# Kernel optimization log

Hardware: AMD Instinct MI355X
Metric: run time of the kernel (lower is better)

Reference implementation:

```python
import jax, jax.numpy as jnp
import numpy as np

BETA1, BETA2, BETA3 = 0.9, 0.8, 0.9
DECAY1, INC1 = 0.05, 5.0
DECAY3, INC3 = 0.05, 5.0
LATENCY = 4.0
B_CONST = 0.15
LIF1_MIN, LIF1_MAX = 150.0, 400.0
LIF3_MIN, LIF3_MAX = 50.0, 200.0
A_P, A_M, TAU_P, TAU_M = 0.01, 0.01, 20.0, 20.0  # exponential STDP params (params1/2/3)


def stdp(dt):
    # exponential STDP curve: potentiate when post fires after pre (dt>=0), depress otherwise
    return jnp.where(dt >= 0, A_P * jnp.exp(-dt / TAU_P), -A_M * jnp.exp(dt / TAU_M))


def setup_inputs() -> dict:
    key = jax.random.key(0)
    k1, k2, k3, k4 = jax.random.split(key, 4)
    H, N, C = 8192, 4096, 128
    return {
        "image": jax.random.uniform(k1, (N,), jnp.float32),
        "W1": jax.random.uniform(k2, (H, N), jnp.float32),
        "W2": jax.random.uniform(k3, (N, H), jnp.float32),
        "W3": jax.random.uniform(k4, (C, N), jnp.float32),
        "thr1": 100.0 * jnp.ones((H,), jnp.float32),
        "thr2": 5.0 * jnp.ones((N,), jnp.float32),
        "thr3": 100.0 * jnp.ones((C,), jnp.float32),
        "time": 256,
        "pw": 8,
    }


def reference(image, W1, W2, W3, thr1, thr2, thr3, time, pw):
    N = image.shape[0]
    H = W1.shape[0]
    C = W3.shape[0]
    T = int(time)
    Tf = jnp.float32(T)

    img_t = Tf * image  # input spike times, [N]
    # rate -> pulse encoding: input_spikes[t, i] = 1 for t in [floor(img_t[i]), floor(img_t[i])+pw)
    t_axis = jnp.arange(T, dtype=jnp.float32)[:, None]          # [T,1]
    start = jnp.floor(img_t)[None, :]                            # [1,N]
    input_spikes = ((t_axis >= start) & (t_axis < start + pw)).astype(jnp.float32)  # [T,N]

    def wta(mem, th):
        # winner-take-all (snntorch inhibition=True): only argmax neuron may spike
        j = jnp.argmax(mem)
        fire = (mem[j] > th[j]).astype(mem.dtype)
        return fire * jax.nn.one_hot(j, mem.shape[0], dtype=mem.dtype)

    def step(carry, xs):
        mem1, mem2, mem3, th1, th3, r1, r2, r3, hid_act, out_act = carry
        x, t = xs
        # layer 1: Leaky LIF, inhibition, reset-to-zero
        mem1 = BETA1 * mem1 + jnp.dot(W1, x)
        spk1 = wta(mem1, th1)
        mem1 = mem1 * (1.0 - spk1)
        # layer 2: Leaky LIF, no inhibition, reset-by-subtract
        mem2 = BETA2 * mem2 + jnp.dot(W2, spk1)
        spk2 = (mem2 > thr2).astype(mem2.dtype)
        mem2 = mem2 - spk2 * thr2
        # layer 3 (clustering): Leaky LIF, inhibition, zeroed after any spike
        mem3 = BETA3 * mem3 + jnp.dot(W3, spk2)
        spk3 = wta(mem3, th3)
        mem3 = mem3 - spk3 * th3
        mem3 = jnp.where(jnp.sum(spk3) > 0, 0.0, mem3)
        # first-spike-time recon (recon stays at first nonzero spk*(t+1))
        r1 = jnp.where(r1 != 0, r1, spk1 * (t + 1.0))
        r2 = jnp.where(r2 != 0, r2, spk2 * (t + 1.0))
        r3 = jnp.where(r3 != 0, r3, spk3 * (t + 1.0))
        hid_act = hid_act + spk1
        out_act = out_act + spk2
        # adaptive thresholds: homeostatic decay + spike-triggered increase, clamped
        th1 = jnp.clip(th1 - DECAY1 + INC1 * spk1, LIF1_MIN, LIF1_MAX)
        th3 = jnp.clip(th3 - DECAY3 + INC3 * spk3, LIF3_MIN, LIF3_MAX)
        return (mem1, mem2, mem3, th1, th3, r1, r2, r3, hid_act, out_act), None

    z = jnp.zeros
    carry0 = (z(H), z(N), z(C), thr1, thr3, z(H), z(N), z(C), z(H), z(N))
    (mem1, mem2, mem3, th1, th3, r1, r2, r3, hid_act, out_act), _ = jax.lax.scan(
        step, carry0, (input_spikes, jnp.arange(T, dtype=jnp.float32)))

    # neurons that never spiked get time T
    r1 = jnp.where(r1 == 0, Tf, r1)
    r2 = jnp.where(r2 == 0, Tf, r2)
    r3 = jnp.where(r3 == 0, Tf, r3)

    # STDP weight updates (exponential), same structure as PresentImage
    hid_mask = (hid_act > 0).astype(jnp.float32)
    delta_t1 = (r1[:, None] - img_t[None, :]) * hid_mask[:, None]      # [H,N]
    W1_new = W1 + stdp(delta_t1)
    delta_t2 = r2[:, None] - r1[None, :]                                # [N,H]
    zeta = (Tf - r1) * hid_mask / Tf                                    # [H]
    rho = (r2 - LATENCY - img_t) / Tf + B_CONST                         # [N]
    W2_new = jnp.clip(W2 + stdp(delta_t2) * (rho[:, None] * zeta[None, :]), 0.0, 1.0)
    delta_t3 = r3[:, None] - r2[None, :]                                # [C,N]
    W3_new = W3 + stdp(delta_t3)

    error = (img_t - (r2 - LATENCY)) / Tf
    error_scalar = jnp.sum(jnp.square(error))
    return (error, error_scalar, r1, r2, r3, W1_new, W2_new, W3_new)
```

## Files before the change

### kernel.cpp

```cpp
#include <hip/hip_runtime.h>
#include <cstdint>
#include <cstddef>

#define Hn 8192
#define Nn 4096
#define Cn 128
#define Tt 256
#define CAP 192

typedef unsigned long long ull;

__device__ __forceinline__ float th_lazy2(float b, float lo, float hi, int nup){
    if (nup <= 0) return b;
    float a = fminf(fmaxf(__fsub_rn(b, 0.05f), lo), hi);
    if (nup == 1) return a;
    return fmaxf(__fsub_rn(a, __fmul_rn(0.05f, (float)(nup - 1))), lo);
}

__device__ __forceinline__ float clamp01(float v){
    return fminf(fmaxf(v, 0.f), 1.f);
}

template<int CTRL>
__device__ __forceinline__ int dpp_i(int x, int old){
    return __builtin_amdgcn_update_dpp(old, x, CTRL, 0xf, 0xf, false);
}
__device__ __forceinline__ float wave_max_f(float v){
    const int NEG = __float_as_int(-3.4e38f);
#define STEPM(C) { float o = __int_as_float(dpp_i<C>(__float_as_int(v), NEG)); v = fmaxf(v, o); }
    STEPM(0x111) STEPM(0x112) STEPM(0x114) STEPM(0x118) STEPM(0x142) STEPM(0x143)
#undef STEPM
    return __int_as_float(__builtin_amdgcn_readlane(__float_as_int(v), 63));
}
__device__ __forceinline__ int wave_argmax_l(float bv, int bh, float &wv, int &wh){
    float v = wave_max_f(bv);
    ull tie = __ballot(bv == v);
    int tl = __ffsll((long long)tie) - 1;
    int h = __builtin_amdgcn_readlane(bh, tl);
    if (__builtin_expect(__popcll(tie) > 1, 0)){
        ull m = tie & (tie - 1);
        while (m){
            int l2 = __ffsll((long long)m) - 1;
            int h2 = __builtin_amdgcn_readlane(bh, l2);
            if (h2 < h){ h = h2; tl = l2; }
            m &= m - 1;
        }
    }
    wv = v; wh = h; return tl;
}
__device__ __forceinline__ float rl_f(float x, int l){
    return __int_as_float(__builtin_amdgcn_readlane(__float_as_int(x), l));
}

__global__ __launch_bounds__(1024) void k_prep(const float* __restrict__ image,
        int* __restrict__ boff, int* __restrict__ sidx, unsigned* __restrict__ anyv){
    __shared__ int s_start[Nn];
    __shared__ int s_c4[4][Tt];
    __shared__ int s_boff[Tt + 1];
    int tid = threadIdx.x;
    for (int i = tid; i < Nn; i += 1024)
        s_start[i] = (int)floorf(__fmul_rn(256.f, image[i]));
    if (tid < Tt) anyv[tid] = 0u;
    __syncthreads();
    int b = tid & 255, q = tid >> 8;
    {
        int c = 0;
        for (int k = 0; k < 1024; ++k) c += (s_start[q * 1024 + k] == b) ? 1 : 0;
        s_c4[q][b] = c;
    }
    __syncthreads();
    if (tid == 0){
        int acc = 0;
        for (int bb = 0; bb < Tt; ++bb){
            s_boff[bb] = acc;
            acc += s_c4[0][bb] + s_c4[1][bb] + s_c4[2][bb] + s_c4[3][bb];
        }
        s_boff[Tt] = acc;
    }
    __syncthreads();
    if (tid <= Tt) boff[tid] = s_boff[tid];
    int p = s_boff[b];
    if (q > 0) p += s_c4[0][b];
    if (q > 1) p += s_c4[1][b];
    if (q > 2) p += s_c4[2][b];
    for (int k = 0; k < 1024; ++k){
        int i = q * 1024 + k;
        if (s_start[i] == b) sidx[p++] = i;
    }
}

__global__ __launch_bounds__(256) void k_gbuckets(const float* __restrict__ W1,
        const int* __restrict__ boff, const int* __restrict__ sidx,
        float* __restrict__ G_T){
    __shared__ float rows[2][Nn];
    int tid = threadIdx.x;
    int h0 = blockIdx.x * 2;
    for (int r = 0; r < 2; ++r){
        const float4* src = (const float4*)(W1 + (size_t)(h0 + r) * Nn);
        float4* dst = (float4*)rows[r];
        for (int j = tid; j < Nn / 4; j += 256) dst[j] = src[j];
    }
    __syncthreads();
    int t = tid;
    int b0 = boff[t], b1 = boff[t + 1];
    float s0 = 0.f, s1 = 0.f;
    for (int k = b0; k < b1; ++k){
        int i = sidx[k];
        s0 += rows[0][i]; s1 += rows[1][i];
    }
    G_T[(size_t)(h0 + 0) * Tt + t] = s0;
    G_T[(size_t)(h0 + 1) * Tt + t] = s1;
}

__global__ __launch_bounds__(256) void k_c1M(const float* __restrict__ G_T,
        float* __restrict__ M, float* __restrict__ r1pre, float* __restrict__ o_r1){
    __shared__ float tile[32][Tt + 1];
    __shared__ float c1s[32][Tt + 1];
    const int tid = threadIdx.x;
    const int h0 = blockIdx.x * 32;
    for (int r = 0; r < 32; ++r) tile[r][tid] = G_T[(size_t)(h0 + r) * Tt + tid];
    __syncthreads();
    {
        int hs = tid & 31, ts = tid >> 5;
        for (int tb = 0; tb < 32; ++tb){
            int t = tb * 8 + ts;
            int lo = (t - 7 < 0) ? 0 : t - 7;
            float s = 0.f;
            for (int u = lo; u <= t; ++u) s += tile[hs][u];
            c1s[hs][t] = s;
        }
    }
    __syncthreads();
    if (tid < 32){
        float m = 0.f;
        for (int t = 0; t < Tt; ++t){
            m = __fadd_rn(__fmul_rn(0.9f, m), c1s[tid][t]);
            M[(size_t)t * Hn + h0 + tid] = m;
        }
        r1pre[h0 + tid] = 0.f;
        o_r1[h0 + tid] = 256.f;
    }
}

__global__ __launch_bounds__(256) void k_sel(const float* __restrict__ M,
        float4* __restrict__ cand){
    const int t = blockIdx.x, tid = threadIdx.x;
    __shared__ float s_row[Hn];
    __shared__ unsigned s_hist[256];
    __shared__ unsigned s_suf[256];
    __shared__ unsigned s_pref;
    __shared__ int s_rank;
    __shared__ int s_cnt;
    __shared__ int s_idx[CAP + 64];
    {
        const float4* src = (const float4*)(M + (size_t)t * Hn);
        float4* d4 = (float4*)s_row;
        for (int j = tid; j < Hn / 4; j += 256) d4[j] = src[j];
    }
    if (tid == 0){ s_pref = 0u; s_rank = CAP; s_cnt = 0; }
    __syncthreads();
#pragma unroll
    for (int b = 3; b >= 0; --b){
        s_hist[tid] = 0u;
        __syncthreads();
        unsigned pref = s_pref;
        int r = s_rank;
        for (int k = 0; k < 32; ++k){
            unsigned u = __float_as_uint(s_row[tid + (k << 8)]);
            bool match = (b == 3) ? true : ((u >> ((b + 1) * 8)) == pref);
            if (match) atomicAdd(&s_hist[(u >> (b * 8)) & 255], 1u);
        }
        __syncthreads();
        s_suf[tid] = s_hist[tid];
        __syncthreads();
#pragma unroll
        for (int off = 1; off < 256; off <<= 1){
            unsigned v = (tid + off < 256) ? s_suf[tid + off] : 0u;
            __syncthreads();
            s_suf[tid] += v;
            __syncthreads();
        }
        unsigned above = s_suf[tid] - s_hist[tid];
        if ((int)above < r && r <= (int)s_suf[tid]){
            s_pref = (pref << 8) | (unsigned)tid;
            s_rank = r - (int)above;
        }
        __syncthreads();
    }
    unsigned V = s_pref;
    for (int k = 0; k < 32; ++k){
        int i = tid + (k << 8);
        unsigned u = __float_as_uint(s_row[i]);
        if (u >= V){
            int p = atomicAdd(&s_cnt, 1);
            if (p < CAP + 64) s_idx[p] = i;
        }
    }
    __syncthreads();
    int c = s_cnt;
    bool ovf = (c > CAP);
    float vV = ovf ? 3.4e38f : __uint_as_float(V);
    for (int i = tid; i < CAP; i += 256){
        float4 e;
        if (!ovf && i < c){
            int ix = s_idx[i];
            e = make_float4(s_row[ix], __int_as_float(ix | (1 << 15)), 0.f, vV);
        } else {
            e = make_float4(-1.f, 0.f, 0.f, vV);
        }
        cand[(size_t)t * CAP + i] = e;
    }
}

#define NB_W1 1024
#define NB_W2 1024
#define NB_W3T 128

union FusedLDS {
    struct {
        float off[Hn];
        float thb[Hn];
        unsigned char ts[Hn];
        int j1[Tt];
        unsigned bm[256];
    } w;
    float tl[64][65];
};

__global__ __launch_bounds__(512, 1) void k_fused(
        const float* __restrict__ M, const float4* __restrict__ cand,
        const float* __restrict__ thr1,
        const float* __restrict__ W1, const float* __restrict__ W2,
        const float* __restrict__ W3,
        float* __restrict__ o_W1, float* __restrict__ o_W2, float* __restrict__ W3T,
        float* __restrict__ r1pre, float* __restrict__ o_r1,
        int* __restrict__ j1s, int* __restrict__ mh, int* __restrict__ nRout){
    __shared__ FusedLDS u;
    const int bid = blockIdx.x;
    const int tid = threadIdx.x;

    if (bid >= 1 && bid < 1 + NB_W1){
        size_t base = (size_t)(bid - 1) * 8192;
        const float4* src = (const float4*)W1;
        float4* dst = (float4*)o_W1;
        for (int i = tid; i < 8192; i += 512){
            float4 s = src[base + i];
            s.x = __fadd_rn(s.x, 0.01f); s.y = __fadd_rn(s.y, 0.01f);
            s.z = __fadd_rn(s.z, 0.01f); s.w = __fadd_rn(s.w, 0.01f);
            dst[base + i] = s;
        }
        return;
    }
    if (bid >= 1 + NB_W1 && bid < 1 + NB_W1 + NB_W2){
        size_t base = (size_t)(bid - 1 - NB_W1) * 8192;
        const float4* src = (const float4*)W2;
        float4* dst = (float4*)o_W2;
        for (int i = tid; i < 8192; i += 512){
            float4 s = src[base + i];
            s.x = clamp01(s.x); s.y = clamp01(s.y);
            s.z = clamp01(s.z); s.w = clamp01(s.w);
            dst[base + i] = s;
        }
        return;
    }
    if (bid >= 1 + NB_W1 + NB_W2){
        int r = bid - 1 - NB_W1 - NB_W2;
        int bx = r & 63, by = r >> 6;
        int n0 = bx * 64, c0 = by * 64;
        for (int e = tid; e < 64 * 64; e += 512){
            int rr = e >> 6, cc = e & 63;
            u.tl[rr][cc] = W3[(size_t)(c0 + rr) * Nn + n0 + cc];
        }
        __syncthreads();
        for (int e = tid; e < 64 * 64; e += 512){
            int rn = e >> 6, cc = e & 63;
            W3T[(size_t)(n0 + rn) * Cn + c0 + cc] = u.tl[cc][rn];
        }
        return;
    }

    for (int h = tid; h < Hn; h += 512){
        u.w.off[h] = 0.f;
        u.w.thb[h] = thr1[h];
        u.w.ts[h] = 0;
    }
    __syncthreads();
    if (tid >= 64) return;
    const int lane = tid;
    const float Lc = -0.15200309344504997f;

    float4 cA0 = cand[lane],         cA1 = cand[64 + lane],         cA2 = cand[128 + lane];
    float4 cB0 = cand[CAP + lane],   cB1 = cand[CAP + 64 + lane],   cB2 = cand[CAP + 128 + lane];
    float4 cC0 = cand[2*CAP + lane], cC1 = cand[2*CAP + 64 + lane], cC2 = cand[2*CAP + 128 + lane];
    float gofA0, gofA1, gofA2, gtsA0, gtsA1, gtsA2, gthA0, gthA1, gthA2;
#define GATHA(c) { int hh = __float_as_int(cA##c.y) & 8191; \
        gofA##c = u.w.off[hh]; gtsA##c = (float)u.w.ts[hh] - 1.f; gthA##c = u.w.thb[hh]; }
    GATHA(0) GATHA(1) GATHA(2)
#undef GATHA

    for (int t = 0; t < Tt; ++t){
        const float tf = (float)t;
        float bm = -3.4e38f; int bhh = 0x7FFFFFFF;
        float braw = 0.f, bts = 0.f, bthb = 0.f;
#define CPROC(c) { \
        int mc = __float_as_int(cA##c.y); \
        int hc = mc & 8191; \
        float dd = __fsub_rn(tf, gtsA##c); \
        float mem = __fsub_rn(cA##c.x, __fmul_rn(exp2f(__fmul_rn(dd, Lc)), gofA##c)); \
        if (!((mc >> 15) & 1)) mem = -3.4e38f; \
        if (mem > bm || (mem == bm && hc < bhh)){ bm = mem; bhh = hc; braw = cA##c.x; bts = gtsA##c; bthb = gthA##c; } }
        CPROC(0) CPROC(1) CPROC(2)
#undef CPROC
        int hB0 = __float_as_int(cB0.y) & 8191;
        int hB1 = __float_as_int(cB1.y) & 8191;
        int hB2 = __float_as_int(cB2.y) & 8191;
        float gofB0 = u.w.off[hB0], gtsB0 = (float)u.w.ts[hB0] - 1.f, gthB0 = u.w.thb[hB0];
        float gofB1 = u.w.off[hB1], gtsB1 = (float)u.w.ts[hB1] - 1.f, gthB1 = u.w.thb[hB1];
        float gofB2 = u.w.off[hB2], gtsB2 = (float)u.w.ts[hB2] - 1.f, gthB2 = u.w.thb[hB2];
        float wv; int wh;
        int wl = wave_argmax_l(bm, bhh, wv, wh);
        float raw = rl_f(braw, wl), tsv = rl_f(bts, wl), thb = rl_f(bthb, wl);
        const float vc = cA0.w;
        int skip = 0;
        if (__builtin_expect(wv < vc, 0)){
            if (t > 0 && vc < 150.f){
                skip = 1;
            } else {
                float fv = -3.4e38f; int fh = 0x7FFFFFFF;
                float fraw = 0.f, fts = 0.f, fthb = 0.f;
                const float4* Mrow4 = (const float4*)(M + (size_t)t * Hn);
                for (int q = 0; q < 32; ++q){
                    int e = q * 64 + lane;
                    float4 mv = Mrow4[e];
                    int ib = e * 4;
#define FPROC(comp, o2) { float x = mv.comp; int h2 = ib + o2; \
                    float gts = (float)u.w.ts[h2] - 1.f; \
                    float dd = __fsub_rn(tf, gts); \
                    float mm = __fsub_rn(x, __fmul_rn(exp2f(__fmul_rn(dd, Lc)), u.w.off[h2])); \
                    if (mm > fv || (mm == fv && h2 < fh)){ fv = mm; fh = h2; fraw = x; fts = gts; fthb = u.w.thb[h2]; } }
                    FPROC(x, 0) FPROC(y, 1) FPROC(z, 2) FPROC(w, 3)
#undef FPROC
                }
                wl = wave_argmax_l(fv, fh, wv, wh);
                raw = rl_f(fraw, wl); tsv = rl_f(fts, wl); fthb = rl_f(fthb, wl); thb = fthb;
            }
        }
        int fire = 0; float thnew = 0.f;
        if (!skip){
            float te = th_lazy2(thb, 150.f, 400.f, t - (int)tsv - 1);
            if (wv > te){
                fire = 1;
                thnew = fminf(fmaxf(__fadd_rn(__fsub_rn(te, 0.05f), 5.0f), 150.f), 400.f);
            }
        }
        if (fire){
            if (lane == 0){
                u.w.j1[t] = wh;
                j1s[t] = wh;
                if (tsv < 0.f){ o_r1[wh] = tf + 1.f; r1pre[wh] = tf + 1.f; }
                u.w.off[wh] = raw;
                u.w.ts[wh] = (unsigned char)((t + 1 < 256) ? (t + 1) : 255);
                u.w.thb[wh] = thnew;
            }
            if (hB0 == wh){ gofB0 = raw; gtsB0 = tf; gthB0 = thnew; }
            if (hB1 == wh){ gofB1 = raw; gtsB1 = tf; gthB1 = thnew; }
            if (hB2 == wh){ gofB2 = raw; gtsB2 = tf; gthB2 = thnew; }
        } else {
            if (lane == 0){ u.w.j1[t] = -1; j1s[t] = -1; }
        }
        cA0 = cB0; cA1 = cB1; cA2 = cB2;
        cB0 = cC0; cB1 = cC1; cB2 = cC2;
        int tn = (t + 3 < Tt) ? t + 3 : Tt - 1;
        cC0 = cand[(size_t)tn * CAP + lane];
        cC1 = cand[(size_t)tn * CAP + 64 + lane];
        cC2 = cand[(size_t)tn * CAP + 128 + lane];
        gofA0 = gofB0; gtsA0 = gtsB0; gthA0 = gthB0;
        gofA1 = gofB1; gtsA1 = gtsB1; gthA1 = gthB1;
        gofA2 = gofB2; gtsA2 = gtsB2; gthA2 = gthB2;
    }

    for (int i = lane; i < 256; i += 64) u.w.bm[i] = 0u;
    asm volatile("s_waitcnt lgkmcnt(0)" ::: "memory");
    for (int i = lane; i < Tt; i += 64){
        int h = u.w.j1[i];
        if (h >= 0) atomicOr(&u.w.bm[h >> 5], 1u << (h & 31));
    }
    asm volatile("s_waitcnt lgkmcnt(0)" ::: "memory");
    unsigned w0 = u.w.bm[lane*4+0], w1 = u.w.bm[lane*4+1];
    unsigned w2 = u.w.bm[lane*4+2], w3 = u.w.bm[lane*4+3];
    int c = __popc(w0) + __popc(w1) + __popc(w2) + __popc(w3);
    int inc = c;
#pragma unroll
    for (int off = 1; off < 64; off <<= 1){
        int v = __shfl_up(inc, off);
        if (lane >= off) inc += v;
    }
    int b = inc - c;
#define WALK(wrd, k) { unsigned ww = wrd; while (ww){ int bt = __ffs(ww) - 1; ww &= ww - 1; \
        mh[b++] = ((lane * 4 + k) << 5) | bt; } }
    WALK(w0, 0) WALK(w1, 1) WALK(w2, 2) WALK(w3, 3)
#undef WALK
    if (lane == 63) *nRout = inc;
}

__global__ __launch_bounds__(64) void k_lif2(const float* __restrict__ W2,
        const int* __restrict__ j1s, const float* __restrict__ thr2,
        float* __restrict__ o_r2, ull* __restrict__ spkb, unsigned* __restrict__ anyv){
    __shared__ int s_j[Tt];
    int lane = threadIdx.x, blk = blockIdx.x;
    for (int i = lane; i < Tt; i += 64) s_j[i] = j1s[i];
    __syncthreads();
    int n = blk * 64 + lane;
    const float* Wrow = W2 + (size_t)n * Hn;
    float tv = thr2[n], m = 0.f, rp = 0.f;
#define LD(dst, tt) { int hh = s_j[tt]; dst = (hh >= 0) ? Wrow[hh] : 0.f; }
#define STEP(uu, tt) { m = __fadd_rn(__fmul_rn(0.8f, m), uu); int f = 0; \
        if (m > tv){ m = __fsub_rn(m, tv); if (rp == 0.f) rp = (float)((tt) + 1); f = 1; } \
        ull mask = __ballot(f); \
        if (lane == 0){ spkb[(tt) * 64 + blk] = mask; if (mask) atomicOr(&anyv[tt], 1u); } }
    float u0, u1, u2, u3;
    LD(u0, 0) LD(u1, 1) LD(u2, 2) LD(u3, 3)
    for (int g = 0; g < 64; ++g){
        float v0 = 0.f, v1 = 0.f, v2 = 0.f, v3 = 0.f;
        if (g < 63){
            int bb = (g + 1) * 4;
            LD(v0, bb) LD(v1, bb + 1) LD(v2, bb + 2) LD(v3, bb + 3)
        }
        int t = g * 4;
        STEP(u0, t) STEP(u1, t + 1) STEP(u2, t + 2) STEP(u3, t + 3)
        u0 = v0; u1 = v1; u2 = v2; u3 = v3;
    }
#undef LD
#undef STEP
    o_r2[n] = (rp == 0.f) ? 256.f : rp;
}

__global__ __launch_bounds__(128, 1) void k_sim3(const ull* __restrict__ spkb,
        const unsigned* __restrict__ anyv, const float* __restrict__ W3T,
        const float* __restrict__ thr3, float* __restrict__ o_r3){
    int tid = threadIdx.x, lane = tid & 63, w = tid >> 6;
    __shared__ unsigned s_any[Tt];
    __shared__ ull s_r2[2];
    __shared__ int s_fire;
    for (int i = tid; i < Tt; i += 128) s_any[i] = anyv[i];
    float m = 0.f, th0 = thr3[tid], rp = 0.f, thv = 0.f;
    int ts = -1, zero = 1;
    __syncthreads();
    for (int t = 0; t < Tt; ++t){
        if (zero && s_any[t] == 0u) continue;
        float d = 0.f;
        if (s_any[t]){
            for (int ww = 0; ww < 64; ++ww){
                ull bits = spkb[t * 64 + ww];
                while (bits){
                    int b2 = __ffsll((long long)bits) - 1;
                    bits &= bits - 1;
                    d = __fadd_rn(d, W3T[(size_t)(ww * 64 + b2) * Cn + tid]);
                }
            }
        }
        m = __fadd_rn(__fmul_rn(0.9f, m), d);
        ull k = (((ull)__float_as_uint(m >= 0.f ? m : 0.f)) << 32) | (unsigned)(8191 - tid);
        if (!(m >= 0.f)) k = (unsigned)(8191 - tid);
#pragma unroll
        for (int off = 32; off >= 1; off >>= 1){
            ull o = __shfl_down(k, off);
            if (o > k) k = o;
        }
        if (lane == 0) s_r2[w] = k;
        __syncthreads();
        ull wk = s_r2[0] > s_r2[1] ? s_r2[0] : s_r2[1];
        int wc = 8191 - (int)(wk & 0xFFFFu);
        float wv = __uint_as_float((unsigned)(wk >> 32));
        if (tid == wc){
            float te = (ts < 0) ? th_lazy2(th0, 50.f, 200.f, t)
                                : th_lazy2(thv, 50.f, 200.f, t - ts - 1);
            int f = (wv > te) ? 1 : 0;
            s_fire = f;
            if (f){
                thv = fminf(fmaxf(__fadd_rn(__fsub_rn(te, 0.05f), 5.0f), 50.f), 200.f);
                ts = t;
                if (rp == 0.f) rp = (float)(t + 1);
            }
        }
        __syncthreads();
        if (s_fire){ m = 0.f; zero = 1; }
        else zero = 0;
        __syncthreads();
    }
    o_r3[tid] = (rp == 0.f) ? 256.f : rp;
}

__global__ __launch_bounds__(1024) void k_scalars(const float* __restrict__ image,
        const float* __restrict__ r1pre, const float* __restrict__ o_r1,
        const float* __restrict__ o_r2,
        float* __restrict__ zeta, float* __restrict__ rho,
        float* __restrict__ imgt, float* __restrict__ eiP, float* __restrict__ eiM,
        float* __restrict__ Pv, float* __restrict__ Qv,
        float* __restrict__ E2P, float* __restrict__ E2M,
        float* __restrict__ o_err, float* __restrict__ o_es){
    int tid = threadIdx.x;
    for (int h = tid; h < Hn; h += 1024){
        float r1f = o_r1[h];
        float mask = (r1pre[h] != 0.f) ? 1.f : 0.f;
        float z = __fmul_rn(__fmul_rn(__fsub_rn(256.f, r1f), mask), 0.00390625f);
        zeta[h] = z;
        Pv[h] = __expf(r1f * 0.05f) * z;
        Qv[h] = __expf(-r1f * 0.05f) * z;
    }
    float acc = 0.f;
    for (int n = tid; n < Nn; n += 1024){
        float img = __fmul_rn(256.f, image[n]);
        float r2f = o_r2[n];
        float e = __fmul_rn(__fsub_rn(img, __fsub_rn(r2f, 4.0f)), 0.00390625f);
        o_err[n] = e;
        rho[n] = __fadd_rn(__fmul_rn(__fsub_rn(__fsub_rn(r2f, 4.0f), img), 0.00390625f), 0.15f);
        imgt[n] = img;
        eiP[n] = __expf(img * 0.05f);
        eiM[n] = __expf(-img * 0.05f);
        E2P[n] = __expf(r2f * 0.05f);
        E2M[n] = __expf(-r2f * 0.05f);
        acc = __fadd_rn(acc, __fmul_rn(e, e));
    }
    __shared__ float red[16];
    for (int off = 32; off >= 1; off >>= 1) acc += __shfl_down(acc, off);
    int lane = tid & 63, w = tid >> 6;
    if (lane == 0) red[w] = acc;
    __syncthreads();
    if (tid == 0){
        float s = 0.f;
        for (int q = 0; q < 16; ++q) s += red[q];
        *o_es = s;
    }
}

__global__ __launch_bounds__(256) void k_w1fix(const float* __restrict__ W1,
        const float* __restrict__ imgt, const float* __restrict__ eiP,
        const float* __restrict__ eiM, const float* __restrict__ o_r1,
        const int* __restrict__ mh, const int* __restrict__ nRout,
        float* __restrict__ o_W1){
    int slot = blockIdx.x;
    if (slot >= *nRout) return;
    int h = mh[slot];
    int tid = threadIdx.x;
    float r1f = o_r1[h];
    float a = 0.01f * __expf(-r1f * 0.05f);
    float b = 0.01f * __expf( r1f * 0.05f);
    const float4* src = (const float4*)(W1 + (size_t)h * Nn);
    float4* dst = (float4*)(o_W1 + (size_t)h * Nn);
    const float4* ig = (const float4*)imgt;
    const float4* p4 = (const float4*)eiP;
    const float4* m4 = (const float4*)eiM;
    for (int i = tid; i < Nn / 4; i += 256){
        float4 s = src[i];
        float4 im = ig[i], pp = p4[i], mm = m4[i];
        s.x += (r1f >= im.x) ? a * pp.x : -(b * mm.x);
        s.y += (r1f >= im.y) ? a * pp.y : -(b * mm.y);
        s.z += (r1f >= im.z) ? a * pp.z : -(b * mm.z);
        s.w += (r1f >= im.w) ? a * pp.w : -(b * mm.w);
        dst[i] = s;
    }
}

__global__ __launch_bounds__(128) void k_w2fix(
        const float* __restrict__ o_r1, const float* __restrict__ Pv,
        const float* __restrict__ Qv, const float* __restrict__ o_r2,
        const float* __restrict__ rho, const int* __restrict__ mh,
        const int* __restrict__ nRout, float* __restrict__ o_W2){
    __shared__ int   s_h[Tt];
    __shared__ float s_rv[Tt], s_pp[Tt], s_qq[Tt];
    int n = blockIdx.x, tid = threadIdx.x;
    int nRv = *nRout;
    for (int s = tid; s < nRv; s += 128){
        int h = mh[s];
        s_h[s] = h; s_rv[s] = o_r1[h]; s_pp[s] = Pv[h]; s_qq[s] = Qv[h];
    }
    __syncthreads();
    float r2f = o_r2[n], rh = rho[n];
    float A = 0.01f * rh * __expf(-r2f * 0.05f);
    float B = 0.01f * rh * __expf( r2f * 0.05f);
    for (int s = tid; s < nRv; s += 128){
        size_t idx = (size_t)n * Hn + s_h[s];
        float w = o_W2[idx];
        float rv = s_rv[s];
        w = clamp01(w + ((r2f >= rv) ? A * s_pp[s] : -(B * s_qq[s])));
        o_W2[idx] = w;
    }
}

__global__ __launch_bounds__(256) void k_w3new(const float* __restrict__ W3,
        const float* __restrict__ o_r2, const float* __restrict__ E2P,
        const float* __restrict__ E2M, const float* __restrict__ o_r3,
        float* __restrict__ o_W3){
    int c = blockIdx.x, tid = threadIdx.x;
    float r3f = o_r3[c];
    float a = 0.01f * __expf(-r3f * 0.05f);
    float b = 0.01f * __expf( r3f * 0.05f);
    const float4* src = (const float4*)(W3 + (size_t)c * Nn);
    float4* dst = (float4*)(o_W3 + (size_t)c * Nn);
    const float4* r24 = (const float4*)o_r2;
    const float4* p4 = (const float4*)E2P;
    const float4* m4 = (const float4*)E2M;
    for (int i = tid; i < Nn / 4; i += 256){
        float4 s = src[i]; float4 rv = r24[i]; float4 pp = p4[i]; float4 mm = m4[i];
        s.x += (r3f >= rv.x) ? a * pp.x : -(b * mm.x);
        s.y += (r3f >= rv.y) ? a * pp.y : -(b * mm.y);
        s.z += (r3f >= rv.z) ? a * pp.z : -(b * mm.z);
        s.w += (r3f >= rv.w) ? a * pp.w : -(b * mm.w);
        dst[i] = s;
    }
}

extern "C" void kernel_launch(void* const* d_in, const int* in_sizes, int n_in,
                              void* d_out, int out_size, void* d_ws, size_t ws_size,
                              hipStream_t stream){
    const float* image = (const float*)d_in[0];
    const float* W1   = (const float*)d_in[1];
    const float* W2   = (const float*)d_in[2];
    const float* W3   = (const float*)d_in[3];
    const float* thr1 = (const float*)d_in[4];
    const float* thr2 = (const float*)d_in[5];
    const float* thr3 = (const float*)d_in[6];

    float* out  = (float*)d_out;
    float* o_err = out;
    float* o_es  = out + 4096;
    float* o_r1  = out + 4097;
    float* o_r2  = out + 12289;
    float* o_r3  = out + 16385;
    float* o_W1  = out + 16513;
    float* o_W2  = o_W1 + (size_t)Hn * Nn;
    float* o_W3  = o_W2 + (size_t)Nn * Hn;

    float* ws = (float*)d_ws;
    float* G_T   = ws;
    float* M     = G_T + (size_t)Hn * Tt;
    float* W3T   = M + (size_t)Tt * Hn;
    float4* cand = (float4*)(W3T + (size_t)Nn * Cn);
    ull* spkb    = (ull*)(cand + (size_t)Tt * CAP);
    float* r1pre = (float*)(spkb + (size_t)Tt * 64);
    float* zeta  = r1pre + Hn;
    float* rho   = zeta + Hn;
    float* imgt  = rho + Nn;
    float* eiP   = imgt + Nn;
    float* eiM   = eiP + Nn;
    float* Pv    = eiM + Nn;
    float* Qv    = Pv + Hn;
    float* E2P   = Qv + Hn;
    float* E2M   = E2P + Nn;
    int* boff   = (int*)(E2M + Nn);
    int* sidx   = boff + (Tt + 1);
    int* j1s    = sidx + Nn;
    int* mh     = j1s + Tt;
    int* nRout  = mh + 256;
    unsigned* anyv = (unsigned*)(nRout + 1);

    k_prep<<<1, 1024, 0, stream>>>(image, boff, sidx, anyv);
    k_gbuckets<<<Hn / 2, 256, 0, stream>>>(W1, boff, sidx, G_T);
    k_c1M<<<Hn / 32, 256, 0, stream>>>(G_T, M, r1pre, o_r1);
    k_sel<<<Tt, 256, 0, stream>>>(M, cand);
    k_fused<<<1 + NB_W1 + NB_W2 + NB_W3T, 512, 0, stream>>>(
        M, cand, thr1, W1, W2, W3, o_W1, o_W2, W3T, r1pre, o_r1, j1s, mh, nRout);
    k_lif2<<<Nn / 64, 64, 0, stream>>>(W2, j1s, thr2, o_r2, spkb, anyv);
    k_sim3<<<1, 128, 0, stream>>>(spkb, anyv, W3T, thr3, o_r3);
    k_scalars<<<1, 1024, 0, stream>>>(image, r1pre, o_r1, o_r2, zeta, rho,
                                      imgt, eiP, eiM, Pv, Qv, E2P, E2M, o_err, o_es);
    k_w1fix<<<256, 256, 0, stream>>>(W1, imgt, eiP, eiM, o_r1, mh, nRout, o_W1);
    k_w2fix<<<Nn, 128, 0, stream>>>(o_r1, Pv, Qv, o_r2, rho, mh, nRout, o_W2);
    k_w3new<<<Cn, 256, 0, stream>>>(W3, o_r2, E2P, E2M, o_r3, o_W3);
}
```

Baseline: 542.1 us.

## Compact layer-1 neuron state into slot-indexed float4 table and shrink fused block

```diff
diff --git a/kernel.cpp b/kernel.cpp
--- a/kernel.cpp
+++ b/kernel.cpp
@@ -143,7 +143,7 @@
 }
 
 __global__ __launch_bounds__(256) void k_sel(const float* __restrict__ M,
-        float4* __restrict__ cand){
+        const float* __restrict__ thr1, float4* __restrict__ cand){
     const int t = blockIdx.x, tid = threadIdx.x;
     __shared__ float s_row[Hn];
     __shared__ unsigned s_hist[256];
@@ -204,7 +204,7 @@
         float4 e;
         if (!ovf && i < c){
             int ix = s_idx[i];
-            e = make_float4(s_row[ix], __int_as_float(ix | (1 << 15)), 0.f, vV);
+            e = make_float4(s_row[ix], __int_as_float(ix | (1 << 15)), thr1[ix], vV);
         } else {
             e = make_float4(-1.f, 0.f, 0.f, vV);
         }
@@ -212,22 +212,21 @@
     }
 }
 
-#define NB_W1 1024
-#define NB_W2 1024
+#define NB_W1 2048
+#define NB_W2 2048
 #define NB_W3T 128
 
 union FusedLDS {
     struct {
-        float off[Hn];
-        float thb[Hn];
-        unsigned char ts[Hn];
+        unsigned short slot[Hn];
+        float4 fst[260];
         int j1[Tt];
         unsigned bm[256];
     } w;
     float tl[64][65];
 };
 
-__global__ __launch_bounds__(512, 1) void k_fused(
+__global__ __launch_bounds__(256, 1) void k_fused(
         const float* __restrict__ M, const float4* __restrict__ cand,
         const float* __restrict__ thr1,
         const float* __restrict__ W1, const float* __restrict__ W2,
@@ -240,10 +239,10 @@
     const int tid = threadIdx.x;
 
     if (bid >= 1 && bid < 1 + NB_W1){
-        size_t base = (size_t)(bid - 1) * 8192;
+        size_t base = (size_t)(bid - 1) * 4096;
         const float4* src = (const float4*)W1;
         float4* dst = (float4*)o_W1;
-        for (int i = tid; i < 8192; i += 512){
+        for (int i = tid; i < 4096; i += 256){
             float4 s = src[base + i];
             s.x = __fadd_rn(s.x, 0.01f); s.y = __fadd_rn(s.y, 0.01f);
             s.z = __fadd_rn(s.z, 0.01f); s.w = __fadd_rn(s.w, 0.01f);
@@ -252,10 +251,10 @@
         return;
     }
     if (bid >= 1 + NB_W1 && bid < 1 + NB_W1 + NB_W2){
-        size_t base = (size_t)(bid - 1 - NB_W1) * 8192;
+        size_t base = (size_t)(bid - 1 - NB_W1) * 4096;
         const float4* src = (const float4*)W2;
         float4* dst = (float4*)o_W2;
-        for (int i = tid; i < 8192; i += 512){
+        for (int i = tid; i < 4096; i += 256){
             float4 s = src[base + i];
             s.x = clamp01(s.x); s.y = clamp01(s.y);
             s.z = clamp01(s.z); s.w = clamp01(s.w);
@@ -267,36 +266,42 @@
         int r = bid - 1 - NB_W1 - NB_W2;
         int bx = r & 63, by = r >> 6;
         int n0 = bx * 64, c0 = by * 64;
-        for (int e = tid; e < 64 * 64; e += 512){
+        for (int e = tid; e < 64 * 64; e += 256){
             int rr = e >> 6, cc = e & 63;
             u.tl[rr][cc] = W3[(size_t)(c0 + rr) * Nn + n0 + cc];
         }
         __syncthreads();
-        for (int e = tid; e < 64 * 64; e += 512){
+        for (int e = tid; e < 64 * 64; e += 256){
             int rn = e >> 6, cc = e & 63;
             W3T[(size_t)(n0 + rn) * Cn + c0 + cc] = u.tl[cc][rn];
         }
         return;
     }
 
-    for (int h = tid; h < Hn; h += 512){
-        u.w.off[h] = 0.f;
-        u.w.thb[h] = thr1[h];
-        u.w.ts[h] = 0;
-    }
+    {
+        uint4 z = make_uint4(0u, 0u, 0u, 0u);
+        uint4* p = (uint4*)u.w.slot;
+        for (int i = tid; i < Hn * 2 / 16; i += 256) p[i] = z;
+    }
+    if (tid == 0) u.w.fst[0] = make_float4(0.f, -1.f, 0.f, 0.f);
     __syncthreads();
     if (tid >= 64) return;
     const int lane = tid;
     const float Lc = -0.15200309344504997f;
+    int nR = 1;
 
     float4 cA0 = cand[lane],         cA1 = cand[64 + lane],         cA2 = cand[128 + lane];
     float4 cB0 = cand[CAP + lane],   cB1 = cand[CAP + 64 + lane],   cB2 = cand[CAP + 128 + lane];
     float4 cC0 = cand[2*CAP + lane], cC1 = cand[2*CAP + 64 + lane], cC2 = cand[2*CAP + 128 + lane];
-    float gofA0, gofA1, gofA2, gtsA0, gtsA1, gtsA2, gthA0, gthA1, gthA2;
-#define GATHA(c) { int hh = __float_as_int(cA##c.y) & 8191; \
-        gofA##c = u.w.off[hh]; gtsA##c = (float)u.w.ts[hh] - 1.f; gthA##c = u.w.thb[hh]; }
-    GATHA(0) GATHA(1) GATHA(2)
-#undef GATHA
+    int slA0, slA1, slA2;
+    float4 stA0, stA1, stA2;
+    {
+        int h0 = __float_as_int(cA0.y) & 8191;
+        int h1 = __float_as_int(cA1.y) & 8191;
+        int h2 = __float_as_int(cA2.y) & 8191;
+        slA0 = u.w.slot[h0]; slA1 = u.w.slot[h1]; slA2 = u.w.slot[h2];
+        stA0 = u.w.fst[slA0]; stA1 = u.w.fst[slA1]; stA2 = u.w.fst[slA2];
+    }
 
     for (int t = 0; t < Tt; ++t){
         const float tf = (float)t;
@@ -305,18 +310,18 @@
 #define CPROC(c) { \
         int mc = __float_as_int(cA##c.y); \
         int hc = mc & 8191; \
-        float dd = __fsub_rn(tf, gtsA##c); \
-        float mem = __fsub_rn(cA##c.x, __fmul_rn(exp2f(__fmul_rn(dd, Lc)), gofA##c)); \
+        float dd = __fsub_rn(tf, stA##c.y); \
+        float mem = __fsub_rn(cA##c.x, __fmul_rn(exp2f(__fmul_rn(dd, Lc)), stA##c.x)); \
+        float thb_c = (slA##c == 0) ? cA##c.z : stA##c.z; \
         if (!((mc >> 15) & 1)) mem = -3.4e38f; \
-        if (mem > bm || (mem == bm && hc < bhh)){ bm = mem; bhh = hc; braw = cA##c.x; bts = gtsA##c; bthb = gthA##c; } }
+        if (mem > bm || (mem == bm && hc < bhh)){ bm = mem; bhh = hc; braw = cA##c.x; bts = stA##c.y; bthb = thb_c; } }
         CPROC(0) CPROC(1) CPROC(2)
 #undef CPROC
         int hB0 = __float_as_int(cB0.y) & 8191;
         int hB1 = __float_as_int(cB1.y) & 8191;
         int hB2 = __float_as_int(cB2.y) & 8191;
-        float gofB0 = u.w.off[hB0], gtsB0 = (float)u.w.ts[hB0] - 1.f, gthB0 = u.w.thb[hB0];
-        float gofB1 = u.w.off[hB1], gtsB1 = (float)u.w.ts[hB1] - 1.f, gthB1 = u.w.thb[hB1];
-        float gofB2 = u.w.off[hB2], gtsB2 = (float)u.w.ts[hB2] - 1.f, gthB2 = u.w.thb[hB2];
+        int slB0 = u.w.slot[hB0], slB1 = u.w.slot[hB1], slB2 = u.w.slot[hB2];
+        float4 stB0 = u.w.fst[slB0], stB1 = u.w.fst[slB1], stB2 = u.w.fst[slB2];
         float wv; int wh;
         int wl = wave_argmax_l(bm, bhh, wv, wh);
         float raw = rl_f(braw, wl), tsv = rl_f(bts, wl), thb = rl_f(bthb, wl);
@@ -334,15 +339,17 @@
                     float4 mv = Mrow4[e];
                     int ib = e * 4;
 #define FPROC(comp, o2) { float x = mv.comp; int h2 = ib + o2; \
-                    float gts = (float)u.w.ts[h2] - 1.f; \
-                    float dd = __fsub_rn(tf, gts); \
-                    float mm = __fsub_rn(x, __fmul_rn(exp2f(__fmul_rn(dd, Lc)), u.w.off[h2])); \
-                    if (mm > fv || (mm == fv && h2 < fh)){ fv = mm; fh = h2; fraw = x; fts = gts; fthb = u.w.thb[h2]; } }
+                    int sl = u.w.slot[h2]; \
+                    float4 st = u.w.fst[sl]; \
+                    float dd = __fsub_rn(tf, st.y); \
+                    float mm = __fsub_rn(x, __fmul_rn(exp2f(__fmul_rn(dd, Lc)), st.x)); \
+                    float tb2 = (sl == 0) ? thr1[h2] : st.z; \
+                    if (mm > fv || (mm == fv && h2 < fh)){ fv = mm; fh = h2; fraw = x; fts = st.y; fthb = tb2; } }
                     FPROC(x, 0) FPROC(y, 1) FPROC(z, 2) FPROC(w, 3)
 #undef FPROC
                 }
                 wl = wave_argmax_l(fv, fh, wv, wh);
-                raw = rl_f(fraw, wl); tsv = rl_f(fts, wl); fthb = rl_f(fthb, wl); thb = fthb;
+                raw = rl_f(fraw, wl); tsv = rl_f(fts, wl); thb = rl_f(fthb, wl);
             }
         }
         int fire = 0; float thnew = 0.f;
@@ -358,13 +365,14 @@
                 u.w.j1[t] = wh;
                 j1s[t] = wh;
                 if (tsv < 0.f){ o_r1[wh] = tf + 1.f; r1pre[wh] = tf + 1.f; }
-                u.w.off[wh] = raw;
-                u.w.ts[wh] = (unsigned char)((t + 1 < 256) ? (t + 1) : 255);
-                u.w.thb[wh] = thnew;
+                u.w.fst[nR] = make_float4(raw, tf, thnew, 0.f);
+                u.w.slot[wh] = (unsigned short)nR;
             }
-            if (hB0 == wh){ gofB0 = raw; gtsB0 = tf; gthB0 = thnew; }
-            if (hB1 == wh){ gofB1 = raw; gtsB1 = tf; gthB1 = thnew; }
-            if (hB2 == wh){ gofB2 = raw; gtsB2 = tf; gthB2 = thnew; }
+            float4 upd = make_float4(raw, tf, thnew, 0.f);
+            if (hB0 == wh){ stB0 = upd; slB0 = nR; }
+            if (hB1 == wh){ stB1 = upd; slB1 = nR; }
+            if (hB2 == wh){ stB2 = upd; slB2 = nR; }
+            nR++;
         } else {
             if (lane == 0){ u.w.j1[t] = -1; j1s[t] = -1; }
         }
@@ -374,9 +382,8 @@
         cC0 = cand[(size_t)tn * CAP + lane];
         cC1 = cand[(size_t)tn * CAP + 64 + lane];
         cC2 = cand[(size_t)tn * CAP + 128 + lane];
-        gofA0 = gofB0; gtsA0 = gtsB0; gthA0 = gthB0;
-        gofA1 = gofB1; gtsA1 = gtsB1; gthA1 = gthB1;
-        gofA2 = gofB2; gtsA2 = gtsB2; gthA2 = gthB2;
+        slA0 = slB0; slA1 = slB1; slA2 = slB2;
+        stA0 = stB0; stA1 = stB1; stA2 = stB2;
     }
 
     for (int i = lane; i < 256; i += 64) u.w.bm[i] = 0u;
@@ -658,8 +665,8 @@
     k_prep<<<1, 1024, 0, stream>>>(image, boff, sidx, anyv);
     k_gbuckets<<<Hn / 2, 256, 0, stream>>>(W1, boff, sidx, G_T);
     k_c1M<<<Hn / 32, 256, 0, stream>>>(G_T, M, r1pre, o_r1);
-    k_sel<<<Tt, 256, 0, stream>>>(M, cand);
-    k_fused<<<1 + NB_W1 + NB_W2 + NB_W3T, 512, 0, stream>>>(
+    k_sel<<<Tt, 256, 0, stream>>>(M, thr1, cand);
+    k_fused<<<1 + NB_W1 + NB_W2 + NB_W3T, 256, 0, stream>>>(
         M, cand, thr1, W1, W2, W3, o_W1, o_W2, W3T, r1pre, o_r1, j1s, mh, nRout);
     k_lif2<<<Nn / 64, 64, 0, stream>>>(W2, j1s, thr2, o_r2, spkb, anyv);
     k_sim3<<<1, 128, 0, stream>>>(spkb, anyv, W3T, thr3, o_r3);
```

Result: slower. 556.1 us (+2.6%).

## Pack per-neuron LIF state into float4 LDS array and unroll weight copy loops

Applied to the files above, without the earlier changes.

```diff
diff --git a/kernel.cpp b/kernel.cpp
--- a/kernel.cpp
+++ b/kernel.cpp
@@ -218,9 +218,7 @@
 
 union FusedLDS {
     struct {
-        float off[Hn];
-        float thb[Hn];
-        unsigned char ts[Hn];
+        float4 mst[Hn];
         int j1[Tt];
         unsigned bm[256];
     } w;
@@ -243,11 +241,23 @@
         size_t base = (size_t)(bid - 1) * 8192;
         const float4* src = (const float4*)W1;
         float4* dst = (float4*)o_W1;
-        for (int i = tid; i < 8192; i += 512){
-            float4 s = src[base + i];
-            s.x = __fadd_rn(s.x, 0.01f); s.y = __fadd_rn(s.y, 0.01f);
-            s.z = __fadd_rn(s.z, 0.01f); s.w = __fadd_rn(s.w, 0.01f);
-            dst[base + i] = s;
+        for (int i = tid; i < 8192; i += 2048){
+            float4 a0 = src[base + i];
+            float4 a1 = src[base + i + 512];
+            float4 a2 = src[base + i + 1024];
+            float4 a3 = src[base + i + 1536];
+            a0.x = __fadd_rn(a0.x, 0.01f); a0.y = __fadd_rn(a0.y, 0.01f);
+            a0.z = __fadd_rn(a0.z, 0.01f); a0.w = __fadd_rn(a0.w, 0.01f);
+            a1.x = __fadd_rn(a1.x, 0.01f); a1.y = __fadd_rn(a1.y, 0.01f);
+            a1.z = __fadd_rn(a1.z, 0.01f); a1.w = __fadd_rn(a1.w, 0.01f);
+            a2.x = __fadd_rn(a2.x, 0.01f); a2.y = __fadd_rn(a2.y, 0.01f);
+            a2.z = __fadd_rn(a2.z, 0.01f); a2.w = __fadd_rn(a2.w, 0.01f);
+            a3.x = __fadd_rn(a3.x, 0.01f); a3.y = __fadd_rn(a3.y, 0.01f);
+            a3.z = __fadd_rn(a3.z, 0.01f); a3.w = __fadd_rn(a3.w, 0.01f);
+            dst[base + i]        = a0;
+            dst[base + i + 512]  = a1;
+            dst[base + i + 1024] = a2;
+            dst[base + i + 1536] = a3;
         }
         return;
     }
@@ -255,11 +265,19 @@
         size_t base = (size_t)(bid - 1 - NB_W1) * 8192;
         const float4* src = (const float4*)W2;
         float4* dst = (float4*)o_W2;
-        for (int i = tid; i < 8192; i += 512){
-            float4 s = src[base + i];
-            s.x = clamp01(s.x); s.y = clamp01(s.y);
-            s.z = clamp01(s.z); s.w = clamp01(s.w);
-            dst[base + i] = s;
+        for (int i = tid; i < 8192; i += 2048){
+            float4 a0 = src[base + i];
+            float4 a1 = src[base + i + 512];
+            float4 a2 = src[base + i + 1024];
+            float4 a3 = src[base + i + 1536];
+            a0.x = clamp01(a0.x); a0.y = clamp01(a0.y); a0.z = clamp01(a0.z); a0.w = clamp01(a0.w);
+            a1.x = clamp01(a1.x); a1.y = clamp01(a1.y); a1.z = clamp01(a1.z); a1.w = clamp01(a1.w);
+            a2.x = clamp01(a2.x); a2.y = clamp01(a2.y); a2.z = clamp01(a2.z); a2.w = clamp01(a2.w);
+            a3.x = clamp01(a3.x); a3.y = clamp01(a3.y); a3.z = clamp01(a3.z); a3.w = clamp01(a3.w);
+            dst[base + i]        = a0;
+            dst[base + i + 512]  = a1;
+            dst[base + i + 1024] = a2;
+            dst[base + i + 1536] = a3;
         }
         return;
     }
@@ -279,11 +297,8 @@
         return;
     }
 
-    for (int h = tid; h < Hn; h += 512){
-        u.w.off[h] = 0.f;
-        u.w.thb[h] = thr1[h];
-        u.w.ts[h] = 0;
-    }
+    for (int h = tid; h < Hn; h += 512)
+        u.w.mst[h] = make_float4(0.f, -1.f, thr1[h], 0.f);
     __syncthreads();
     if (tid >= 64) return;
     const int lane = tid;
@@ -292,11 +307,13 @@
     float4 cA0 = cand[lane],         cA1 = cand[64 + lane],         cA2 = cand[128 + lane];
     float4 cB0 = cand[CAP + lane],   cB1 = cand[CAP + 64 + lane],   cB2 = cand[CAP + 128 + lane];
     float4 cC0 = cand[2*CAP + lane], cC1 = cand[2*CAP + 64 + lane], cC2 = cand[2*CAP + 128 + lane];
-    float gofA0, gofA1, gofA2, gtsA0, gtsA1, gtsA2, gthA0, gthA1, gthA2;
-#define GATHA(c) { int hh = __float_as_int(cA##c.y) & 8191; \
-        gofA##c = u.w.off[hh]; gtsA##c = (float)u.w.ts[hh] - 1.f; gthA##c = u.w.thb[hh]; }
-    GATHA(0) GATHA(1) GATHA(2)
-#undef GATHA
+    float4 gA0, gA1, gA2;
+    {
+        int h0 = __float_as_int(cA0.y) & 8191;
+        int h1 = __float_as_int(cA1.y) & 8191;
+        int h2 = __float_as_int(cA2.y) & 8191;
+        gA0 = u.w.mst[h0]; gA1 = u.w.mst[h1]; gA2 = u.w.mst[h2];
+    }
 
     for (int t = 0; t < Tt; ++t){
         const float tf = (float)t;
@@ -305,18 +322,18 @@
 #define CPROC(c) { \
         int mc = __float_as_int(cA##c.y); \
         int hc = mc & 8191; \
-        float dd = __fsub_rn(tf, gtsA##c); \
-        float mem = __fsub_rn(cA##c.x, __fmul_rn(exp2f(__fmul_rn(dd, Lc)), gofA##c)); \
+        float dd = __fsub_rn(tf, gA##c.y); \
+        float mem = __fsub_rn(cA##c.x, __fmul_rn(exp2f(__fmul_rn(dd, Lc)), gA##c.x)); \
         if (!((mc >> 15) & 1)) mem = -3.4e38f; \
-        if (mem > bm || (mem == bm && hc < bhh)){ bm = mem; bhh = hc; braw = cA##c.x; bts = gtsA##c; bthb = gthA##c; } }
+        if (mem > bm || (mem == bm && hc < bhh)){ bm = mem; bhh = hc; braw = cA##c.x; bts = gA##c.y; bthb = gA##c.z; } }
         CPROC(0) CPROC(1) CPROC(2)
 #undef CPROC
-        int hB0 = __float_as_int(cB0.y) & 8191;
-        int hB1 = __float_as_int(cB1.y) & 8191;
-        int hB2 = __float_as_int(cB2.y) & 8191;
-        float gofB0 = u.w.off[hB0], gtsB0 = (float)u.w.ts[hB0] - 1.f, gthB0 = u.w.thb[hB0];
-        float gofB1 = u.w.off[hB1], gtsB1 = (float)u.w.ts[hB1] - 1.f, gthB1 = u.w.thb[hB1];
-        float gofB2 = u.w.off[hB2], gtsB2 = (float)u.w.ts[hB2] - 1.f, gthB2 = u.w.thb[hB2];
+        const int hB0 = __float_as_int(cB0.y) & 8191;
+        const int hB1 = __float_as_int(cB1.y) & 8191;
+        const int hB2 = __float_as_int(cB2.y) & 8191;
+        float4 gB0 = u.w.mst[hB0];
+        float4 gB1 = u.w.mst[hB1];
+        float4 gB2 = u.w.mst[hB2];
         float wv; int wh;
         int wl = wave_argmax_l(bm, bhh, wv, wh);
         float raw = rl_f(braw, wl), tsv = rl_f(bts, wl), thb = rl_f(bthb, wl);
@@ -333,16 +350,16 @@
                     int e = q * 64 + lane;
                     float4 mv = Mrow4[e];
                     int ib = e * 4;
-#define FPROC(comp, o2) { float x = mv.comp; int h2 = ib + o2; \
-                    float gts = (float)u.w.ts[h2] - 1.f; \
-                    float dd = __fsub_rn(tf, gts); \
-                    float mm = __fsub_rn(x, __fmul_rn(exp2f(__fmul_rn(dd, Lc)), u.w.off[h2])); \
-                    if (mm > fv || (mm == fv && h2 < fh)){ fv = mm; fh = h2; fraw = x; fts = gts; fthb = u.w.thb[h2]; } }
-                    FPROC(x, 0) FPROC(y, 1) FPROC(z, 2) FPROC(w, 3)
+                    float4 g0 = u.w.mst[ib+0], g1 = u.w.mst[ib+1], g2 = u.w.mst[ib+2], g3 = u.w.mst[ib+3];
+#define FPROC(comp, gg, o2) { float x = mv.comp; float dd = __fsub_rn(tf, gg.y); \
+                    float mm = __fsub_rn(x, __fmul_rn(exp2f(__fmul_rn(dd, Lc)), gg.x)); \
+                    int h2 = ib + o2; \
+                    if (mm > fv || (mm == fv && h2 < fh)){ fv = mm; fh = h2; fraw = x; fts = gg.y; fthb = gg.z; } }
+                    FPROC(x, g0, 0) FPROC(y, g1, 1) FPROC(z, g2, 2) FPROC(w, g3, 3)
 #undef FPROC
                 }
                 wl = wave_argmax_l(fv, fh, wv, wh);
-                raw = rl_f(fraw, wl); tsv = rl_f(fts, wl); fthb = rl_f(fthb, wl); thb = fthb;
+                raw = rl_f(fraw, wl); tsv = rl_f(fts, wl); thb = rl_f(fthb, wl);
             }
         }
         int fire = 0; float thnew = 0.f;
@@ -356,17 +373,15 @@
         if (fire){
             if (lane == 0){
                 u.w.j1[t] = wh;
-                j1s[t] = wh;
                 if (tsv < 0.f){ o_r1[wh] = tf + 1.f; r1pre[wh] = tf + 1.f; }
-                u.w.off[wh] = raw;
-                u.w.ts[wh] = (unsigned char)((t + 1 < 256) ? (t + 1) : 255);
-                u.w.thb[wh] = thnew;
+                u.w.mst[wh] = make_float4(raw, tf, thnew, 0.f);
             }
-            if (hB0 == wh){ gofB0 = raw; gtsB0 = tf; gthB0 = thnew; }
-            if (hB1 == wh){ gofB1 = raw; gtsB1 = tf; gthB1 = thnew; }
-            if (hB2 == wh){ gofB2 = raw; gtsB2 = tf; gthB2 = thnew; }
+            float4 upd = make_float4(raw, tf, thnew, 0.f);
+            if (hB0 == wh) gB0 = upd;
+            if (hB1 == wh) gB1 = upd;
+            if (hB2 == wh) gB2 = upd;
         } else {
-            if (lane == 0){ u.w.j1[t] = -1; j1s[t] = -1; }
+            if (lane == 0) u.w.j1[t] = -1;
         }
         cA0 = cB0; cA1 = cB1; cA2 = cB2;
         cB0 = cC0; cB1 = cC1; cB2 = cC2;
@@ -374,15 +389,14 @@
         cC0 = cand[(size_t)tn * CAP + lane];
         cC1 = cand[(size_t)tn * CAP + 64 + lane];
         cC2 = cand[(size_t)tn * CAP + 128 + lane];
-        gofA0 = gofB0; gtsA0 = gtsB0; gthA0 = gthB0;
-        gofA1 = gofB1; gtsA1 = gtsB1; gthA1 = gthB1;
-        gofA2 = gofB2; gtsA2 = gtsB2; gthA2 = gthB2;
+        gA0 = gB0; gA1 = gB1; gA2 = gB2;
     }
 
     for (int i = lane; i < 256; i += 64) u.w.bm[i] = 0u;
     asm volatile("s_waitcnt lgkmcnt(0)" ::: "memory");
     for (int i = lane; i < Tt; i += 64){
         int h = u.w.j1[i];
+        j1s[i] = h;
         if (h >= 0) atomicOr(&u.w.bm[h >> 5], 1u << (h & 31));
     }
     asm volatile("s_waitcnt lgkmcnt(0)" ::: "memory");
```

Result: faster. 506.8 us (-6.5%).
